# Performance work log

Measured on AMD Instinct MI355X. Metric: run time of the kernel, lower is better.

Reference implementation:

```python
import jax, jax.numpy as jnp
import numpy as np

N = 100000
E = 1600000
B = 64
NUM_CLASSES = 10


def setup_inputs() -> dict:
    key = jax.random.key(0)
    ks = jax.random.split(key, 8)
    x = jax.random.normal(ks[0], (N, 5), dtype=jnp.float32)
    edge_index = jax.random.randint(ks[1], (2, E), 0, N, dtype=jnp.int64)
    batch = jnp.sort(jax.random.randint(ks[2], (N,), 0, B, dtype=jnp.int64))

    def glorot(k, fan_in, fan_out):
        s = jnp.sqrt(6.0 / (fan_in + fan_out)).astype(jnp.float32)
        return jax.random.uniform(k, (fan_in, fan_out), jnp.float32, -s, s)

    dims = [(5, 32), (32, 64), (64, 128), (128, 256)]
    Ws = [glorot(jax.random.fold_in(ks[3], i), a, b) for i, (a, b) in enumerate(dims)]
    bs = [jnp.zeros((b,), jnp.float32) for (_, b) in dims]
    fc1_w = glorot(ks[4], 256, 100)
    fc1_b = jnp.zeros((100,), jnp.float32)
    fc2_w = glorot(ks[5], 100, NUM_CLASSES)
    fc2_b = jnp.zeros((NUM_CLASSES,), jnp.float32)
    return {
        'x': x, 'edge_index': edge_index, 'batch': batch,
        'W1': Ws[0], 'b1': bs[0], 'W2': Ws[1], 'b2': bs[1],
        'W3': Ws[2], 'b3': bs[2], 'W4': Ws[3], 'b4': bs[3],
        'fc1_w': fc1_w, 'fc1_b': fc1_b, 'fc2_w': fc2_w, 'fc2_b': fc2_b,
    }


def _gcn_conv(x, W, b, src, dst, dinv):
    h = x @ W                                   # [N, out]
    norm = (dinv[src] * dinv[dst])[:, None]      # [E, 1]
    msg = h[src] * norm                          # gather + scale
    agg = jax.ops.segment_sum(msg, dst, num_segments=N)
    agg = agg + h * (dinv * dinv)[:, None]       # self-loop contribution
    return agg + b


def reference(x, edge_index, batch, W1, b1, W2, b2, W3, b3, W4, b4,
              fc1_w, fc1_b, fc2_w, fc2_b):
    src, dst = edge_index[0], edge_index[1]
    # degree including self-loop
    deg = jax.ops.segment_sum(jnp.ones((E,), jnp.float32), dst, num_segments=N) + 1.0
    dinv = jax.lax.rsqrt(deg)

    h = jax.nn.relu(_gcn_conv(x, W1, b1, src, dst, dinv))
    # mesh_unpool with pool target 0 -> identity
    h = jax.nn.relu(_gcn_conv(h, W2, b2, src, dst, dinv))
    h = jax.nn.relu(_gcn_conv(h, W3, b3, src, dst, dinv))
    h = jax.nn.relu(_gcn_conv(h, W4, b4, src, dst, dinv))

    # global mean pool over graphs
    sums = jax.ops.segment_sum(h, batch, num_segments=B)
    cnt = jax.ops.segment_sum(jnp.ones((N,), jnp.float32), batch, num_segments=B)
    pooled = sums / jnp.maximum(cnt, 1.0)[:, None]

    h = jax.nn.relu(pooled @ fc1_w + fc1_b)
    return jax.nn.log_softmax(h @ fc2_w + fc2_b, axis=-1)
```

## Files before the change

### kernel.cpp

```cpp
#include <hip/hip_runtime.h>
#include <hip/hip_bf16.h>
#include <cmath>

#define NN 100000
#define NE 1600000
#define NBATCH 64
#define NB 391
#define NBP 512
#define BCAP 6144
#define NPAD (NB * BCAP)

typedef __attribute__((ext_vector_type(8))) _Float16 f16x8;
typedef __attribute__((ext_vector_type(4))) float f32x4;
typedef __attribute__((ext_vector_type(2))) float f32x2;
typedef __attribute__((ext_vector_type(4))) unsigned int u32x4;

__device__ __forceinline__ void atomAdd(float* p, float v) {
  unsafeAtomicAdd(p, v);
}

__device__ __forceinline__ unsigned char f2fp8(float f) {
  int pk = __builtin_amdgcn_cvt_pk_fp8_f32(f, f, 0, false);
  return (unsigned char)(pk & 0xff);
}

__device__ __forceinline__ u32x4 ldnt(const u32x4* p) {
  return __builtin_nontemporal_load(p);
}

__device__ __forceinline__ void acc16(uint4 v, f32x2* acc) {
  acc[0] += __builtin_amdgcn_cvt_pk_f32_fp8(v.x, false);
  acc[1] += __builtin_amdgcn_cvt_pk_f32_fp8(v.x, true);
  acc[2] += __builtin_amdgcn_cvt_pk_f32_fp8(v.y, false);
  acc[3] += __builtin_amdgcn_cvt_pk_f32_fp8(v.y, true);
  acc[4] += __builtin_amdgcn_cvt_pk_f32_fp8(v.z, false);
  acc[5] += __builtin_amdgcn_cvt_pk_f32_fp8(v.z, true);
  acc[6] += __builtin_amdgcn_cvt_pk_f32_fp8(v.w, false);
  acc[7] += __builtin_amdgcn_cvt_pk_f32_fp8(v.w, true);
}

__global__ __launch_bounds__(256) void k_bin(const int* __restrict__ src,
    const int* __restrict__ dst, int* __restrict__ bucketCnt, unsigned* __restrict__ pairs,
    const float* __restrict__ W2, const float* __restrict__ W3, const float* __restrict__ W4,
    _Float16* __restrict__ Wt2, _Float16* __restrict__ Wt3, _Float16* __restrict__ Wt4) {
  __shared__ int hist[NBP];
  __shared__ int scn[NBP];
  __shared__ int ofs[NBP];
  __shared__ int gbase[NBP];
  __shared__ unsigned buf[4096];
  __shared__ unsigned short bufb[4096];
  const int base = blockIdx.x * 4096;
  const int n = (NE - base < 4096) ? NE - base : 4096;
  for (int i = threadIdx.x; i < NBP; i += 256) hist[i] = 0;
  __syncthreads();

  int myS[16], myD[16];
  int nloc = 0;
  for (int i = threadIdx.x, j = 0; i < n; i += 256, ++j) {
    myS[j] = src[base + i];
    myD[j] = dst[base + i];
    atomicAdd(&hist[myD[j] >> 8], 1);
    nloc = j + 1;
  }
  __syncthreads();

  scn[threadIdx.x] = hist[threadIdx.x];
  scn[threadIdx.x + 256] = hist[threadIdx.x + 256];
  __syncthreads();
  for (int off = 1; off < NBP; off <<= 1) {
    const int i0 = threadIdx.x, i1 = threadIdx.x + 256;
    int t0 = (i0 >= off) ? scn[i0 - off] : 0;
    int t1 = (i1 >= off) ? scn[i1 - off] : 0;
    __syncthreads();
    scn[i0] += t0;
    scn[i1] += t1;
    __syncthreads();
  }
  ofs[threadIdx.x] = scn[threadIdx.x] - hist[threadIdx.x];
  ofs[threadIdx.x + 256] = scn[threadIdx.x + 256] - hist[threadIdx.x + 256];
  for (int b = threadIdx.x; b < NB; b += 256) {
    int c = hist[b];
    if (c) gbase[b] = b * BCAP + atomicAdd(&bucketCnt[b], c);
  }
  __syncthreads();

  for (int j = 0; j < nloc; ++j) {
    int b = myD[j] >> 8;
    int slot = atomicAdd(&ofs[b], 1);
    buf[slot] = ((unsigned)myS[j] << 8) | ((unsigned)myD[j] & 255u);
    bufb[slot] = (unsigned short)b;
  }
  __syncthreads();

  for (int i = threadIdx.x; i < n; i += 256) {
    int b = (int)bufb[i];
    int ex = scn[b] - hist[b];
    pairs[gbase[b] + (i - ex)] = buf[i];
  }

  int idx = blockIdx.x * 256 + threadIdx.x;
  if (idx < 2048) {
    int k = idx / 64, m = idx - k * 64;
    Wt2[m * 32 + k] = (_Float16)W2[idx];
  } else if (idx < 10240) {
    int j = idx - 2048;
    int k = j / 128, m = j - k * 128;
    Wt3[m * 64 + k] = (_Float16)W3[j];
  } else if (idx < 43008) {
    int j = idx - 10240;
    int k = j / 256, m = j - k * 256;
    Wt4[m * 128 + k] = (_Float16)W4[j];
  }
}

__global__ __launch_bounds__(256) void k_cntfill(const unsigned* __restrict__ pairs,
    const int* __restrict__ bucketCnt, const int* __restrict__ batch,
    const float* __restrict__ x, int* __restrict__ rowbeg, int* __restrict__ rowend,
    float* __restrict__ dinv, int* __restrict__ csrc, float* __restrict__ pcnt,
    _Float16* __restrict__ xs8, unsigned char* __restrict__ F0,
    unsigned char* __restrict__ F1, unsigned char* __restrict__ F2) {
  __shared__ int c[256];
  __shared__ int scn[256];
  __shared__ int rowb[256];
  __shared__ int ofs[256];
  __shared__ int h[64];
  const int tid = threadIdx.x;
  c[tid] = 0; ofs[tid] = 0;
  if (tid < 64) h[tid] = 0;
  __syncthreads();
  const int b = blockIdx.x;
  const int s = b * BCAP;
  const int e = s + bucketCnt[b];
  for (int i = s + tid; i < e; i += 256) atomicAdd(&c[pairs[i] & 255u], 1);
  __syncthreads();
  const int v = c[tid];
  const int pv = (v + 3) & ~3;
  scn[tid] = pv;
  __syncthreads();
  for (int off = 1; off < 256; off <<= 1) {
    int t = (tid >= off) ? scn[tid - off] : 0;
    __syncthreads();
    scn[tid] += t;
    __syncthreads();
  }
  rowb[tid] = s + scn[tid] - pv;
  const int node = b * 256 + tid;
  rowbeg[node] = rowb[tid];
  rowend[node] = rowb[tid] + v;
  for (int p = v; p < pv; ++p) csrc[rowb[tid] + p] = NN;
  if (node < NN) {
    const float di = rsqrtf((float)v + 1.0f);
    dinv[node] = di;
    f16x8 o = {0, 0, 0, 0, 0, 0, 0, 0};
    o[0] = (_Float16)(x[(size_t)node * 5 + 0] * di);
    o[1] = (_Float16)(x[(size_t)node * 5 + 1] * di);
    o[2] = (_Float16)(x[(size_t)node * 5 + 2] * di);
    o[3] = (_Float16)(x[(size_t)node * 5 + 3] * di);
    o[4] = (_Float16)(x[(size_t)node * 5 + 4] * di);
    *(f16x8*)(xs8 + (size_t)node * 8) = o;
    atomicAdd(&h[batch[node]], 1);
  }
  if (b == 0 && tid < 15) {
    const uint4 z = make_uint4(0u, 0u, 0u, 0u);
    if (tid < 1)      ((uint4*)(xs8 + (size_t)NN * 8))[tid] = z;
    else if (tid < 3) ((uint4*)(F0 + (size_t)NN * 32))[tid - 1] = z;
    else if (tid < 7) ((uint4*)(F1 + (size_t)NN * 64))[tid - 3] = z;
    else              ((uint4*)(F2 + (size_t)NN * 128))[tid - 7] = z;
  }
  __syncthreads();
  for (int i = s + tid; i < e; i += 256) {
    unsigned p = pairs[i];
    int t = (int)(p & 255u);
    int pos = rowb[t] + atomicAdd(&ofs[t], 1);
    csrc[pos] = (int)(p >> 8);
  }
  if (tid < 64 && h[tid]) atomAdd(&pcnt[tid], (float)h[tid]);
}

struct MegaArgs {
  const _Float16* xs8;
  const int* rowbeg; const int* rowend; const int* csrc;
  const float* dinv;
  const float* W1; const float* b1;
  unsigned char* F0;
  const _Float16* Wt2; const float* b2;
  unsigned char* F1;
  const _Float16* Wt3; const float* b3;
  unsigned char* F2;
  const _Float16* Wt4; const float* b4;
  const int* batch; float* pooled; const float* pcnt;
  const float* fc1w; const float* fc1b; const float* fc2w; const float* fc2b;
  float* out;
};

__global__ __launch_bounds__(256) void kw_l1(MegaArgs a) {
  __shared__ float w_s[160];
  __shared__ float b_s[32];
  const int tid = threadIdx.x;
  if (tid < 160) w_s[tid] = a.W1[tid];
  if (tid < 32) b_s[tid] = a.b1[tid];
  __syncthreads();
  const int r = blockIdx.x * 256 + tid;
  if (r >= NN) return;
  const float di = a.dinv[r];
  const _Float16* xs = a.xs8;
  f16x8 av = *(const f16x8*)(xs + (size_t)r * 8);
  f16x8 a0 = {0,0,0,0,0,0,0,0}, a1 = {0,0,0,0,0,0,0,0};
  f16x8 a2 = {0,0,0,0,0,0,0,0}, a3 = {0,0,0,0,0,0,0,0};
  const int eb = a.rowbeg[r];
  const int nIt = (a.rowend[r] - eb + 3) >> 2;
  const u32x4* cp = (const u32x4*)(a.csrc + eb);
  u32x4 i0 = ldnt(cp), i1 = ldnt(cp + 1);
  int it = 0;
  for (; it + 2 <= nIt; it += 2) {
    const f16x8 f0 = *(const f16x8*)(xs + (size_t)i0.x * 8);
    const f16x8 f1 = *(const f16x8*)(xs + (size_t)i0.y * 8);
    const f16x8 f2 = *(const f16x8*)(xs + (size_t)i0.z * 8);
    const f16x8 f3 = *(const f16x8*)(xs + (size_t)i0.w * 8);
    const f16x8 f4 = *(const f16x8*)(xs + (size_t)i1.x * 8);
    const f16x8 f5 = *(const f16x8*)(xs + (size_t)i1.y * 8);
    const f16x8 f6 = *(const f16x8*)(xs + (size_t)i1.z * 8);
    const f16x8 f7 = *(const f16x8*)(xs + (size_t)i1.w * 8);
    const u32x4 n0 = ldnt(cp + it + 2), n1 = ldnt(cp + it + 3);
    a0 += f0; a1 += f1; a2 += f2; a3 += f3;
    a0 += f4; a1 += f5; a2 += f6; a3 += f7;
    i0 = n0; i1 = n1;
  }
  if (it < nIt) {
    const f16x8 f0 = *(const f16x8*)(xs + (size_t)i0.x * 8);
    const f16x8 f1 = *(const f16x8*)(xs + (size_t)i0.y * 8);
    const f16x8 f2 = *(const f16x8*)(xs + (size_t)i0.z * 8);
    const f16x8 f3 = *(const f16x8*)(xs + (size_t)i0.w * 8);
    a0 += f0; a1 += f1; a2 += f2; a3 += f3;
  }
  a0 += a1; a2 += a3; a0 += a2; av += a0;
  const float f0 = (float)av[0] * di, f1 = (float)av[1] * di, f2 = (float)av[2] * di,
              f3 = (float)av[3] * di, f4 = (float)av[4] * di;
  float v[32];
#pragma unroll
  for (int j = 0; j < 32; ++j) {
    float s = b_s[j] + f0 * w_s[j] + f1 * w_s[32 + j] + f2 * w_s[64 + j]
                     + f3 * w_s[96 + j] + f4 * w_s[128 + j];
    v[j] = fmaxf(s, 0.f) * di;
  }
  unsigned u[8];
#pragma unroll
  for (int g2 = 0; g2 < 8; ++g2) {
    int uu = 0;
    uu = __builtin_amdgcn_cvt_pk_fp8_f32(v[4 * g2],     v[4 * g2 + 1], uu, false);
    uu = __builtin_amdgcn_cvt_pk_fp8_f32(v[4 * g2 + 2], v[4 * g2 + 3], uu, true);
    u[g2] = (unsigned)uu;
  }
  uint4* op = (uint4*)(a.F0 + (size_t)r * 32);
  op[0] = make_uint4(u[0], u[1], u[2], u[3]);
  op[1] = make_uint4(u[4], u[5], u[6], u[7]);
}

template<int K, int M, int BROWS, int MODE, int THREADS>
__global__ __launch_bounds__(THREADS) void kw_fgemm(MegaArgs a,
    const unsigned char* __restrict__ in,
    const _Float16* __restrict__ Wt, const float* __restrict__ bias,
    unsigned char* __restrict__ outp) {
  constexpr int KC = 32;
  constexpr int KP = K + 8;
  constexpr int NW = THREADS / 64;
  constexpr int MW = M / NW;
  constexpr int CTW = MW / 16;
  constexpr int RT = BROWS / 16;
  constexpr int TPR = K / 16;
  constexpr int RPP = THREADS / TPR;
  constexpr int NPASS = (BROWS + RPP - 1) / RPP;
  __shared__ _Float16 a_s[BROWS * KP];
  const int tid = threadIdx.x;
  const int wave = tid >> 6, lane = tid & 63;
  const int m16 = lane & 15, q = lane >> 4;
  const int r0 = blockIdx.x * BROWS;

  {
    const int rowg = tid / TPR;
    const int c = (tid % TPR) * 16;
    const unsigned char* bp = in + c;
#pragma unroll
    for (int pass = 0; pass < NPASS; ++pass) {
      const int row = pass * RPP + rowg;
      if (NPASS > 1 && row >= BROWS) break;
      const int r = r0 + row;
      f32x2 acc8[8];
#pragma unroll
      for (int i = 0; i < 8; ++i) acc8[i] = (f32x2){0.f, 0.f};
      float di = 0.f;
      if (r < NN) {
        di = a.dinv[r];
        const int eb = a.rowbeg[r];
        const int nIt = (a.rowend[r] - eb + 3) >> 2;
        const u32x4* cp = (const u32x4*)(a.csrc + eb);
        u32x4 i0 = ldnt(cp), i1 = ldnt(cp + 1);
        acc16(*(const uint4*)(bp + (size_t)r * K), acc8);
        int it = 0;
        for (; it + 2 <= nIt; it += 2) {
          const uint4 f0 = *(const uint4*)(bp + (size_t)i0.x * K);
          const uint4 f1 = *(const uint4*)(bp + (size_t)i0.y * K);
          const uint4 f2 = *(const uint4*)(bp + (size_t)i0.z * K);
          const uint4 f3 = *(const uint4*)(bp + (size_t)i0.w * K);
          const uint4 f4 = *(const uint4*)(bp + (size_t)i1.x * K);
          const uint4 f5 = *(const uint4*)(bp + (size_t)i1.y * K);
          const uint4 f6 = *(const uint4*)(bp + (size_t)i1.z * K);
          const uint4 f7 = *(const uint4*)(bp + (size_t)i1.w * K);
          const u32x4 n0 = ldnt(cp + it + 2), n1 = ldnt(cp + it + 3);
          acc16(f0, acc8); acc16(f1, acc8); acc16(f2, acc8); acc16(f3, acc8);
          acc16(f4, acc8); acc16(f5, acc8); acc16(f6, acc8); acc16(f7, acc8);
          i0 = n0; i1 = n1;
        }
        if (it < nIt) {
          const uint4 f0 = *(const uint4*)(bp + (size_t)i0.x * K);
          const uint4 f1 = *(const uint4*)(bp + (size_t)i0.y * K);
          const uint4 f2 = *(const uint4*)(bp + (size_t)i0.z * K);
          const uint4 f3 = *(const uint4*)(bp + (size_t)i0.w * K);
          acc16(f0, acc8); acc16(f1, acc8); acc16(f2, acc8); acc16(f3, acc8);
        }
      }
      _Float16 h[16];
#pragma unroll
      for (int i = 0; i < 8; ++i) {
        h[2 * i]     = (_Float16)(acc8[i].x * di);
        h[2 * i + 1] = (_Float16)(acc8[i].y * di);
      }
      *(uint4*)&a_s[row * KP + c]     = *(uint4*)&h[0];
      *(uint4*)&a_s[row * KP + c + 8] = *(uint4*)&h[8];
    }
  }
  __syncthreads();

  f32x4 acc[RT][CTW];
#pragma unroll
  for (int rt = 0; rt < RT; ++rt)
#pragma unroll
    for (int ct = 0; ct < CTW; ++ct) acc[rt][ct] = (f32x4){0.f, 0.f, 0.f, 0.f};

  const _Float16* wp = Wt + (size_t)(wave * MW) * K + q * 8;
#pragma unroll
  for (int kc = 0; kc < K; kc += KC) {
    f16x8 bfr[CTW];
#pragma unroll
    for (int ct = 0; ct < CTW; ++ct)
      bfr[ct] = *(const f16x8*)(wp + (size_t)(ct * 16 + m16) * K + kc);
#pragma unroll
    for (int rt = 0; rt < RT; ++rt) {
      f16x8 afr = *(const f16x8*)&a_s[(rt * 16 + m16) * KP + kc + q * 8];
#pragma unroll
      for (int ct = 0; ct < CTW; ++ct)
        acc[rt][ct] = __builtin_amdgcn_mfma_f32_16x16x32_f16(afr, bfr[ct], acc[rt][ct], 0, 0, 0);
    }
  }

  if constexpr (MODE == 1) {
    const int rlast = (r0 + BROWS - 1 < NN) ? r0 + BROWS - 1 : NN - 1;
    const int bmin = a.batch[r0];
    const int bmax = a.batch[rlast];
    int rowb[RT][4];
#pragma unroll
    for (int rt = 0; rt < RT; ++rt)
#pragma unroll
      for (int reg = 0; reg < 4; ++reg) {
        const int row = r0 + rt * 16 + q * 4 + reg;
        rowb[rt][reg] = (row < NN) ? a.batch[row] : -1;
      }
#pragma unroll
    for (int ct = 0; ct < CTW; ++ct) {
      const int col = wave * MW + ct * 16 + m16;
      const float bv = bias[col];
      for (int b = bmin; b <= bmax; ++b) {
        float s = 0.f;
#pragma unroll
        for (int rt = 0; rt < RT; ++rt)
#pragma unroll
          for (int reg = 0; reg < 4; ++reg)
            if (rowb[rt][reg] == b) s += fmaxf(acc[rt][ct][reg] + bv, 0.f);
        s += __shfl_xor(s, 16);
        s += __shfl_xor(s, 32);
        if (q == 0) atomAdd(&a.pooled[b * M + col], s);
      }
    }
  } else {
#pragma unroll
    for (int rt = 0; rt < RT; ++rt) {
#pragma unroll
      for (int ct = 0; ct < CTW; ++ct) {
        const int col = wave * MW + ct * 16 + m16;
        const float bv = bias[col];
#pragma unroll
        for (int reg = 0; reg < 4; ++reg) {
          const int row = r0 + rt * 16 + q * 4 + reg;
          if (row < NN) {
            float vv = fmaxf(acc[rt][ct][reg] + bv, 0.f) * a.dinv[row];
            outp[(size_t)row * M + col] = f2fp8(vv);
          }
        }
      }
    }
  }
}

__global__ __launch_bounds__(256) void kw_mlp(MegaArgs a) {
  __shared__ float p[256];
  __shared__ float h1[100];
  __shared__ float lo[10];
  const int tid = threadIdx.x;
  const int b = blockIdx.x;
  const float inv = 1.0f / fmaxf(a.pcnt[b], 1.0f);
  p[tid] = a.pooled[b * 256 + tid] * inv;
  __syncthreads();
  for (int j = tid; j < 100; j += 256) {
    float s = a.fc1b[j];
    for (int k = 0; k < 256; ++k) s += p[k] * a.fc1w[k * 100 + j];
    h1[j] = fmaxf(s, 0.f);
  }
  __syncthreads();
  if (tid < 10) {
    float s = a.fc2b[tid];
    for (int k = 0; k < 100; ++k) s += h1[k] * a.fc2w[k * 10 + tid];
    lo[tid] = s;
  }
  __syncthreads();
  if (tid == 0) {
    float m = lo[0];
    for (int j = 1; j < 10; ++j) m = fmaxf(m, lo[j]);
    float ssum = 0.f;
    for (int j = 0; j < 10; ++j) ssum += expf(lo[j] - m);
    float lse = m + logf(ssum);
    for (int j = 0; j < 10; ++j) a.out[b * 10 + j] = lo[j] - lse;
  }
}

extern "C" void kernel_launch(void* const* d_in, const int* in_sizes, int n_in,
                              void* d_out, int out_size, void* d_ws, size_t ws_size,
                              hipStream_t stream) {
  const float* x     = (const float*)d_in[0];
  const int*   ei    = (const int*)d_in[1];
  const int*   batch = (const int*)d_in[2];
  const float* W1 = (const float*)d_in[3];  const float* b1 = (const float*)d_in[4];
  const float* W2 = (const float*)d_in[5];  const float* b2 = (const float*)d_in[6];
  const float* W3 = (const float*)d_in[7];  const float* b3 = (const float*)d_in[8];
  const float* W4 = (const float*)d_in[9];  const float* b4 = (const float*)d_in[10];
  const float* fc1w = (const float*)d_in[11]; const float* fc1b = (const float*)d_in[12];
  const float* fc2w = (const float*)d_in[13]; const float* fc2b = (const float*)d_in[14];
  float* out = (float*)d_out;

  const int* src = ei;
  const int* dst = ei + NE;

  float* ws = (float*)d_ws;
  float* pooled = ws;
  float* pcnt   = pooled + 16384;
  int*   bucketCnt = (int*)(pcnt + 64);
  float* dinv   = (float*)(bucketCnt + 512);
  int*   rowbeg = (int*)(dinv + 100352);
  int*   rowend = rowbeg + 100352;
  int*   csrc   = rowend + 100352;
  unsigned* pairs = (unsigned*)(csrc + NPAD);
  _Float16* xs8 = (_Float16*)(pairs + NPAD);
  unsigned char* F0 = (unsigned char*)(xs8 + 800768);
  unsigned char* F1 = F0 + 3200128;
  unsigned char* F2 = F1 + 6400128;
  _Float16* Wt2 = (_Float16*)(F2 + 12800128);
  _Float16* Wt3 = Wt2 + 32 * 64;
  _Float16* Wt4 = Wt3 + 64 * 128;

  (void)hipMemsetAsync(pooled, 0, (16384 + 64 + 512) * sizeof(float), stream);
  k_bin<<<(NE + 4095) / 4096, 256, 0, stream>>>(src, dst, bucketCnt, pairs,
                                                W2, W3, W4, Wt2, Wt3, Wt4);
  k_cntfill<<<NB, 256, 0, stream>>>(pairs, bucketCnt, batch, x,
                                    rowbeg, rowend, dinv, csrc, pcnt, xs8,
                                    F0, F1, F2);

  MegaArgs m;
  m.xs8 = xs8; m.rowbeg = rowbeg; m.rowend = rowend; m.csrc = csrc;
  m.dinv = dinv;
  m.W1 = W1; m.b1 = b1; m.F0 = F0;
  m.Wt2 = Wt2; m.b2 = b2; m.F1 = F1;
  m.Wt3 = Wt3; m.b3 = b3; m.F2 = F2;
  m.Wt4 = Wt4; m.b4 = b4;
  m.batch = batch; m.pooled = pooled; m.pcnt = pcnt;
  m.fc1w = fc1w; m.fc1b = fc1b; m.fc2w = fc2w; m.fc2b = fc2b;
  m.out = out;

  kw_l1<<<(NN + 255) / 256, 256, 0, stream>>>(m);
  kw_fgemm<32, 64, 64, 0, 128><<<(NN + 63) / 64, 128, 0, stream>>>(m, F0, Wt2, b2, F1);
  kw_fgemm<64, 128, 64, 0, 256><<<(NN + 63) / 64, 256, 0, stream>>>(m, F1, Wt3, b3, F2);
  kw_fgemm<128, 256, 64, 1, 512><<<(NN + 63) / 64, 512, 0, stream>>>(m, F2, Wt4, b4, nullptr);
  kw_mlp<<<NBATCH, 256, 0, stream>>>(m);
}
```

Measured before the change: 277.0 us.

## Split per-row edge gathers across lane groups with shuffle reduction

Layer 1 and the first two fused gather-GEMM layers now assign several lanes per destination row, each walking an interleaved slice of the CSR edge list. Partial sums are combined with xor-shuffles before the transform and the fp8/fp16 store. The aim is more memory-level parallelism and less load imbalance from long rows in the latency-bound gathers. It costs extra threads and shuffles, and layers 2-3 get smaller row tiles, which changes GEMM tile reuse.

```diff
diff --git a/kernel.cpp b/kernel.cpp
--- a/kernel.cpp
+++ b/kernel.cpp
@@ -200,63 +200,72 @@
   if (tid < 160) w_s[tid] = a.W1[tid];
   if (tid < 32) b_s[tid] = a.b1[tid];
   __syncthreads();
-  const int r = blockIdx.x * 256 + tid;
+  const int gid = blockIdx.x * 256 + tid;
+  const int r = gid >> 2;
+  const int eg = gid & 3;
   if (r >= NN) return;
   const float di = a.dinv[r];
   const _Float16* xs = a.xs8;
-  f16x8 av = *(const f16x8*)(xs + (size_t)r * 8);
+  f16x8 av = {0,0,0,0,0,0,0,0};
+  if (eg == 0) av = *(const f16x8*)(xs + (size_t)r * 8);
   f16x8 a0 = {0,0,0,0,0,0,0,0}, a1 = {0,0,0,0,0,0,0,0};
   f16x8 a2 = {0,0,0,0,0,0,0,0}, a3 = {0,0,0,0,0,0,0,0};
   const int eb = a.rowbeg[r];
   const int nIt = (a.rowend[r] - eb + 3) >> 2;
-  const u32x4* cp = (const u32x4*)(a.csrc + eb);
-  u32x4 i0 = ldnt(cp), i1 = ldnt(cp + 1);
-  int it = 0;
-  for (; it + 2 <= nIt; it += 2) {
-    const f16x8 f0 = *(const f16x8*)(xs + (size_t)i0.x * 8);
-    const f16x8 f1 = *(const f16x8*)(xs + (size_t)i0.y * 8);
-    const f16x8 f2 = *(const f16x8*)(xs + (size_t)i0.z * 8);
-    const f16x8 f3 = *(const f16x8*)(xs + (size_t)i0.w * 8);
-    const f16x8 f4 = *(const f16x8*)(xs + (size_t)i1.x * 8);
-    const f16x8 f5 = *(const f16x8*)(xs + (size_t)i1.y * 8);
-    const f16x8 f6 = *(const f16x8*)(xs + (size_t)i1.z * 8);
-    const f16x8 f7 = *(const f16x8*)(xs + (size_t)i1.w * 8);
-    const u32x4 n0 = ldnt(cp + it + 2), n1 = ldnt(cp + it + 3);
-    a0 += f0; a1 += f1; a2 += f2; a3 += f3;
-    a0 += f4; a1 += f5; a2 += f6; a3 += f7;
-    i0 = n0; i1 = n1;
-  }
-  if (it < nIt) {
-    const f16x8 f0 = *(const f16x8*)(xs + (size_t)i0.x * 8);
-    const f16x8 f1 = *(const f16x8*)(xs + (size_t)i0.y * 8);
-    const f16x8 f2 = *(const f16x8*)(xs + (size_t)i0.z * 8);
-    const f16x8 f3 = *(const f16x8*)(xs + (size_t)i0.w * 8);
-    a0 += f0; a1 += f1; a2 += f2; a3 += f3;
+  const int nL = (nIt - eg + 3) >> 2;
+  if (nL > 0) {
+    const u32x4* cp = (const u32x4*)(a.csrc + eb) + eg;
+    u32x4 i0 = ldnt(cp), i1 = ldnt(cp + 4);
+    int k = 0;
+    for (; k + 2 <= nL; k += 2) {
+      const f16x8 f0 = *(const f16x8*)(xs + (size_t)i0.x * 8);
+      const f16x8 f1 = *(const f16x8*)(xs + (size_t)i0.y * 8);
+      const f16x8 f2 = *(const f16x8*)(xs + (size_t)i0.z * 8);
+      const f16x8 f3 = *(const f16x8*)(xs + (size_t)i0.w * 8);
+      const f16x8 f4 = *(const f16x8*)(xs + (size_t)i1.x * 8);
+      const f16x8 f5 = *(const f16x8*)(xs + (size_t)i1.y * 8);
+      const f16x8 f6 = *(const f16x8*)(xs + (size_t)i1.z * 8);
+      const f16x8 f7 = *(const f16x8*)(xs + (size_t)i1.w * 8);
+      const u32x4 n0 = ldnt(cp + (k + 2) * 4), n1 = ldnt(cp + (k + 3) * 4);
+      a0 += f0; a1 += f1; a2 += f2; a3 += f3;
+      a0 += f4; a1 += f5; a2 += f6; a3 += f7;
+      i0 = n0; i1 = n1;
+    }
+    if (k < nL) {
+      const f16x8 f0 = *(const f16x8*)(xs + (size_t)i0.x * 8);
+      const f16x8 f1 = *(const f16x8*)(xs + (size_t)i0.y * 8);
+      const f16x8 f2 = *(const f16x8*)(xs + (size_t)i0.z * 8);
+      const f16x8 f3 = *(const f16x8*)(xs + (size_t)i0.w * 8);
+      a0 += f0; a1 += f1; a2 += f2; a3 += f3;
+    }
   }
   a0 += a1; a2 += a3; a0 += a2; av += a0;
-  const float f0 = (float)av[0] * di, f1 = (float)av[1] * di, f2 = (float)av[2] * di,
-              f3 = (float)av[3] * di, f4 = (float)av[4] * di;
-  float v[32];
-#pragma unroll
-  for (int j = 0; j < 32; ++j) {
+  float f0 = (float)av[0], f1 = (float)av[1], f2 = (float)av[2],
+        f3 = (float)av[3], f4 = (float)av[4];
+  f0 += __shfl_xor(f0, 1); f0 += __shfl_xor(f0, 2);
+  f1 += __shfl_xor(f1, 1); f1 += __shfl_xor(f1, 2);
+  f2 += __shfl_xor(f2, 1); f2 += __shfl_xor(f2, 2);
+  f3 += __shfl_xor(f3, 1); f3 += __shfl_xor(f3, 2);
+  f4 += __shfl_xor(f4, 1); f4 += __shfl_xor(f4, 2);
+  f0 *= di; f1 *= di; f2 *= di; f3 *= di; f4 *= di;
+  float v[8];
+  const int j0 = eg * 8;
+#pragma unroll
+  for (int jj = 0; jj < 8; ++jj) {
+    const int j = j0 + jj;
     float s = b_s[j] + f0 * w_s[j] + f1 * w_s[32 + j] + f2 * w_s[64 + j]
                      + f3 * w_s[96 + j] + f4 * w_s[128 + j];
-    v[j] = fmaxf(s, 0.f) * di;
-  }
-  unsigned u[8];
-#pragma unroll
-  for (int g2 = 0; g2 < 8; ++g2) {
-    int uu = 0;
-    uu = __builtin_amdgcn_cvt_pk_fp8_f32(v[4 * g2],     v[4 * g2 + 1], uu, false);
-    uu = __builtin_amdgcn_cvt_pk_fp8_f32(v[4 * g2 + 2], v[4 * g2 + 3], uu, true);
-    u[g2] = (unsigned)uu;
-  }
-  uint4* op = (uint4*)(a.F0 + (size_t)r * 32);
-  op[0] = make_uint4(u[0], u[1], u[2], u[3]);
-  op[1] = make_uint4(u[4], u[5], u[6], u[7]);
-}
-
-template<int K, int M, int BROWS, int MODE, int THREADS>
+    v[jj] = fmaxf(s, 0.f) * di;
+  }
+  int u0 = 0, u1 = 0;
+  u0 = __builtin_amdgcn_cvt_pk_fp8_f32(v[0], v[1], u0, false);
+  u0 = __builtin_amdgcn_cvt_pk_fp8_f32(v[2], v[3], u0, true);
+  u1 = __builtin_amdgcn_cvt_pk_fp8_f32(v[4], v[5], u1, false);
+  u1 = __builtin_amdgcn_cvt_pk_fp8_f32(v[6], v[7], u1, true);
+  *(uint2*)(a.F0 + (size_t)r * 32 + j0) = make_uint2((unsigned)u0, (unsigned)u1);
+}
+
+template<int K, int M, int BROWS, int MODE, int THREADS, int EG>
 __global__ __launch_bounds__(THREADS) void kw_fgemm(MegaArgs a,
     const unsigned char* __restrict__ in,
     const _Float16* __restrict__ Wt, const float* __restrict__ bias,
@@ -268,7 +277,8 @@
   constexpr int CTW = MW / 16;
   constexpr int RT = BROWS / 16;
   constexpr int TPR = K / 16;
-  constexpr int RPP = THREADS / TPR;
+  constexpr int LPR = TPR * EG;
+  constexpr int RPP = THREADS / LPR;
   constexpr int NPASS = (BROWS + RPP - 1) / RPP;
   __shared__ _Float16 a_s[BROWS * KP];
   const int tid = threadIdx.x;
@@ -277,8 +287,10 @@
   const int r0 = blockIdx.x * BROWS;
 
   {
-    const int rowg = tid / TPR;
-    const int c = (tid % TPR) * 16;
+    const int rowg = tid / LPR;
+    const int sub = tid % LPR;
+    const int eg = sub / TPR;
+    const int c = (sub % TPR) * 16;
     const unsigned char* bp = in + c;
 #pragma unroll
     for (int pass = 0; pass < NPASS; ++pass) {
@@ -293,40 +305,55 @@
         di = a.dinv[r];
         const int eb = a.rowbeg[r];
         const int nIt = (a.rowend[r] - eb + 3) >> 2;
-        const u32x4* cp = (const u32x4*)(a.csrc + eb);
-        u32x4 i0 = ldnt(cp), i1 = ldnt(cp + 1);
-        acc16(*(const uint4*)(bp + (size_t)r * K), acc8);
-        int it = 0;
-        for (; it + 2 <= nIt; it += 2) {
-          const uint4 f0 = *(const uint4*)(bp + (size_t)i0.x * K);
-          const uint4 f1 = *(const uint4*)(bp + (size_t)i0.y * K);
-          const uint4 f2 = *(const uint4*)(bp + (size_t)i0.z * K);
-          const uint4 f3 = *(const uint4*)(bp + (size_t)i0.w * K);
-          const uint4 f4 = *(const uint4*)(bp + (size_t)i1.x * K);
-          const uint4 f5 = *(const uint4*)(bp + (size_t)i1.y * K);
-          const uint4 f6 = *(const uint4*)(bp + (size_t)i1.z * K);
-          const uint4 f7 = *(const uint4*)(bp + (size_t)i1.w * K);
-          const u32x4 n0 = ldnt(cp + it + 2), n1 = ldnt(cp + it + 3);
-          acc16(f0, acc8); acc16(f1, acc8); acc16(f2, acc8); acc16(f3, acc8);
-          acc16(f4, acc8); acc16(f5, acc8); acc16(f6, acc8); acc16(f7, acc8);
-          i0 = n0; i1 = n1;
-        }
-        if (it < nIt) {
-          const uint4 f0 = *(const uint4*)(bp + (size_t)i0.x * K);
-          const uint4 f1 = *(const uint4*)(bp + (size_t)i0.y * K);
-          const uint4 f2 = *(const uint4*)(bp + (size_t)i0.z * K);
-          const uint4 f3 = *(const uint4*)(bp + (size_t)i0.w * K);
-          acc16(f0, acc8); acc16(f1, acc8); acc16(f2, acc8); acc16(f3, acc8);
+        if (eg == 0) acc16(*(const uint4*)(bp + (size_t)r * K), acc8);
+        const int nL = (EG == 1) ? nIt : (nIt - eg + EG - 1) / EG;
+        if (nL > 0) {
+          const u32x4* cp = (const u32x4*)(a.csrc + eb) + eg;
+          u32x4 i0 = ldnt(cp), i1 = ldnt(cp + EG);
+          int k = 0;
+          for (; k + 2 <= nL; k += 2) {
+            const uint4 f0 = *(const uint4*)(bp + (size_t)i0.x * K);
+            const uint4 f1 = *(const uint4*)(bp + (size_t)i0.y * K);
+            const uint4 f2 = *(const uint4*)(bp + (size_t)i0.z * K);
+            const uint4 f3 = *(const uint4*)(bp + (size_t)i0.w * K);
+            const uint4 f4 = *(const uint4*)(bp + (size_t)i1.x * K);
+            const uint4 f5 = *(const uint4*)(bp + (size_t)i1.y * K);
+            const uint4 f6 = *(const uint4*)(bp + (size_t)i1.z * K);
+            const uint4 f7 = *(const uint4*)(bp + (size_t)i1.w * K);
+            const u32x4 n0 = ldnt(cp + (k + 2) * EG), n1 = ldnt(cp + (k + 3) * EG);
+            acc16(f0, acc8); acc16(f1, acc8); acc16(f2, acc8); acc16(f3, acc8);
+            acc16(f4, acc8); acc16(f5, acc8); acc16(f6, acc8); acc16(f7, acc8);
+            i0 = n0; i1 = n1;
+          }
+          if (k < nL) {
+            const uint4 f0 = *(const uint4*)(bp + (size_t)i0.x * K);
+            const uint4 f1 = *(const uint4*)(bp + (size_t)i0.y * K);
+            const uint4 f2 = *(const uint4*)(bp + (size_t)i0.z * K);
+            const uint4 f3 = *(const uint4*)(bp + (size_t)i0.w * K);
+            acc16(f0, acc8); acc16(f1, acc8); acc16(f2, acc8); acc16(f3, acc8);
+          }
         }
       }
-      _Float16 h[16];
-#pragma unroll
-      for (int i = 0; i < 8; ++i) {
-        h[2 * i]     = (_Float16)(acc8[i].x * di);
-        h[2 * i + 1] = (_Float16)(acc8[i].y * di);
+      if (EG > 1) {
+#pragma unroll
+        for (int msk = TPR; msk < LPR; msk <<= 1) {
+#pragma unroll
+          for (int i = 0; i < 8; ++i) {
+            acc8[i].x += __shfl_xor(acc8[i].x, msk);
+            acc8[i].y += __shfl_xor(acc8[i].y, msk);
+          }
+        }
       }
-      *(uint4*)&a_s[row * KP + c]     = *(uint4*)&h[0];
-      *(uint4*)&a_s[row * KP + c + 8] = *(uint4*)&h[8];
+      if (EG == 1 || (sub / TPR) == 0) {
+        _Float16 h[16];
+#pragma unroll
+        for (int i = 0; i < 8; ++i) {
+          h[2 * i]     = (_Float16)(acc8[i].x * di);
+          h[2 * i + 1] = (_Float16)(acc8[i].y * di);
+        }
+        *(uint4*)&a_s[row * KP + c]     = *(uint4*)&h[0];
+        *(uint4*)&a_s[row * KP + c + 8] = *(uint4*)&h[8];
+      }
     }
   }
   __syncthreads();
@@ -484,9 +511,9 @@
   m.fc1w = fc1w; m.fc1b = fc1b; m.fc2w = fc2w; m.fc2b = fc2b;
   m.out = out;
 
-  kw_l1<<<(NN + 255) / 256, 256, 0, stream>>>(m);
-  kw_fgemm<32, 64, 64, 0, 128><<<(NN + 63) / 64, 128, 0, stream>>>(m, F0, Wt2, b2, F1);
-  kw_fgemm<64, 128, 64, 0, 256><<<(NN + 63) / 64, 256, 0, stream>>>(m, F1, Wt3, b3, F2);
-  kw_fgemm<128, 256, 64, 1, 512><<<(NN + 63) / 64, 512, 0, stream>>>(m, F2, Wt4, b4, nullptr);
+  kw_l1<<<(NN * 4 + 255) / 256, 256, 0, stream>>>(m);
+  kw_fgemm<32, 64, 32, 0, 256, 4><<<(NN + 31) / 32, 256, 0, stream>>>(m, F0, Wt2, b2, F1);
+  kw_fgemm<64, 128, 32, 0, 256, 2><<<(NN + 31) / 32, 256, 0, stream>>>(m, F1, Wt3, b3, F2);
+  kw_fgemm<128, 256, 64, 1, 512, 1><<<(NN + 63) / 64, 512, 0, stream>>>(m, F2, Wt4, b4, nullptr);
   kw_mlp<<<NBATCH, 256, 0, stream>>>(m);
 }
```

Result: faster. 266.6 us, median of 2 (-3.7%).
